# Performance work log

Measured on AMD Instinct MI355X. Metric: run time of the kernel, lower is better.

## Reference

```python
import jax, jax.numpy as jnp
import numpy as np

B, N, D, H = 4, 1024, 512, 16
DH = D // H
FACTOR = 0.5 / np.sqrt(DH).astype(np.float32)


def setup_inputs() -> dict:
    key = jax.random.key(0)
    ks = jax.random.split(key, 16)
    w = lambda k, shape: (jax.random.normal(k, shape, dtype=jnp.float32) * 0.02)
    return {
        "H": jax.random.normal(ks[0], (B, N, D), dtype=jnp.float32),
        "V": jax.random.normal(ks[1], (B, N, 3, D), dtype=jnp.float32),
        "D_batch": jax.random.normal(ks[2], (B, N, N), dtype=jnp.float32),
        "rbf_feat": jax.random.normal(ks[3], (1, B, H, N, N), dtype=jnp.float32),
        "H_mask": jax.random.randint(ks[4], (B, N), 0, 2).astype(jnp.int32),
        "Wq": w(ks[5], (4 * D, D)), "bq": w(ks[6], (4 * D,)),
        "Wk": w(ks[7], (4 * D, D)), "bk": w(ks[8], (4 * D,)),
        "Wv": w(ks[9], (D, D)), "bv": w(ks[10], (D,)),
        "Wvv": w(ks[11], (D, D)),
        "Wo": w(ks[12], (D, D)), "bo": w(ks[13], (D,)),
        "Wvo": w(ks[14], (D, D)),
    }


def reference(H, V, D_batch, rbf_feat, H_mask, Wq, bq, Wk, bk, Wv, bv, Wvv, Wo, bo, Wvo):
    b, n, d = H.shape
    h = rbf_feat.shape[2]
    dh = d // h
    # projections
    H_q = (H @ Wq.T + bq).reshape(b, n, h, 4 * dh)
    H_k = (H @ Wk.T + bk).reshape(b, n, h, 4 * dh)
    H_v = (H @ Wv.T + bv).reshape(b, n, h, dh)
    # vector values: [b,n,3,d] -> [b,n,3,h,dh] -> [b,n,h,3,dh] -> [b,n,h,3*dh]
    V_v = jnp.einsum('bncd,ed->bnce', V, Wvv)
    V_v = jnp.swapaxes(V_v.reshape(b, n, 3, h, dh), -2, -3).reshape(b, n, h, 3 * dh)
    V_attn = jnp.concatenate([H_v, V_v], axis=-1)  # [b,n,h,4*dh]
    # additive bias + key mask
    bias = rbf_feat[0] + D_batch[:, None]            # [b,h,n,n]
    mask = (H_mask[:, None, None, :] != 0)           # [b,1,1,n]
    bias = jnp.where(mask, bias, -jnp.inf)
    scores = jnp.einsum('bnhd,bmhd->bhnm', H_q, H_k) * jnp.float32(FACTOR) + bias
    attn = jax.nn.softmax(scores, axis=-1)
    res = jnp.einsum('bhnm,bmhd->bnhd', attn, V_attn)  # [b,n,h,4*dh]
    H_res = res[..., :dh].reshape(b, n, d)
    V_res = jnp.swapaxes(res[..., dh:].reshape(b, n, h, 3, dh), -2, -3).reshape(b, n, 3, d)
    H_o = H_res @ Wo.T + bo
    V_o = jnp.einsum('bncd,ed->bnce', V_res, Wvo)
    return (H_o, V_o)
```

## Files before the change

### kernel.cpp

```cpp
#include <hip/hip_runtime.h>
#include <cmath>

#define FACTOR 0.08838834764831845f

typedef short s16x8 __attribute__((ext_vector_type(8)));
typedef float f32x4 __attribute__((ext_vector_type(4)));
typedef float f32x16 __attribute__((ext_vector_type(16)));
typedef unsigned int u32;

#define KEEP_LOADS() do { asm volatile("" ::: "memory"); __builtin_amdgcn_sched_barrier(0); } while (0)

__device__ __forceinline__ unsigned short f2bf(float x) {
  unsigned int u = __float_as_uint(x);
  u += 0x7FFFu + ((u >> 16) & 1u);
  return (unsigned short)(u >> 16);
}

__device__ __forceinline__ s16x8 pack8(float4 a, float4 b) {
  s16x8 r;
  r[0] = (short)f2bf(a.x); r[1] = (short)f2bf(a.y);
  r[2] = (short)f2bf(a.z); r[3] = (short)f2bf(a.w);
  r[4] = (short)f2bf(b.x); r[5] = (short)f2bf(b.y);
  r[6] = (short)f2bf(b.z); r[7] = (short)f2bf(b.w);
  return r;
}

__device__ __forceinline__ void gload_lds16(const void* g, void* l) {
  __builtin_amdgcn_global_load_lds(
      (const __attribute__((address_space(1))) u32*)g,
      (__attribute__((address_space(3))) u32*)l, 16, 0, 0);
}

__global__ __launch_bounds__(256) void gemm_mfma(
    const float* __restrict__ A, const float* __restrict__ B,
    const float* __restrict__ bias, void* __restrict__ C,
    int M, int N, int K, int mode)
{
  __shared__ unsigned short As[128 * 72];
  __shared__ unsigned short Bs[128 * 72];

  const int tid = threadIdx.x;
  const int w = tid >> 6, lane = tid & 63;
  const int l16 = lane & 15, lg = lane >> 4;
  const int wm = w >> 1, wn = w & 1;
  const int m0 = blockIdx.x * 128;
  const int n0 = blockIdx.y * 128;

  const int sr = tid >> 3;
  const int sc = (tid & 7) * 8;

  float4 ar[4][2], br[4][2];

  auto issue = [&](int k0) {
#pragma unroll
    for (int i = 0; i < 4; ++i) {
      const int rr = i * 32 + sr;
      const float* ap = A + (size_t)(m0 + rr) * K + k0 + sc;
      ar[i][0] = *(const float4*)ap;
      ar[i][1] = *(const float4*)(ap + 4);
      const float* bp;
      if (mode == 5) {
        const int t = n0 + rr;
        const int q3 = t >> 10, n = t & 1023;
        const int bb = q3 / 3, cd = q3 - 3 * bb;
        bp = B + (((size_t)(bb * 1024 + n)) * 3 + cd) * 512 + k0 + sc;
      } else {
        bp = B + (size_t)(n0 + rr) * K + k0 + sc;
      }
      br[i][0] = *(const float4*)bp;
      br[i][1] = *(const float4*)(bp + 4);
    }
  };

  f32x4 acc[4][4];
#pragma unroll
  for (int mt = 0; mt < 4; ++mt)
#pragma unroll
    for (int nt = 0; nt < 4; ++nt)
#pragma unroll
      for (int r = 0; r < 4; ++r) acc[mt][nt][r] = 0.f;

  issue(0);

#pragma unroll 1
  for (int k0 = 0; k0 < K; k0 += 64) {
    __builtin_amdgcn_s_barrier();
#pragma unroll
    for (int i = 0; i < 4; ++i) {
      const int rr = i * 32 + sr;
      *(s16x8*)&As[rr * 72 + sc] = pack8(ar[i][0], ar[i][1]);
      *(s16x8*)&Bs[rr * 72 + sc] = pack8(br[i][0], br[i][1]);
    }
    asm volatile("s_waitcnt lgkmcnt(0)" ::: "memory");
    __builtin_amdgcn_s_barrier();
    if (k0 + 64 < K) issue(k0 + 64);
    KEEP_LOADS();

#pragma unroll
    for (int ks = 0; ks < 2; ++ks) {
      s16x8 af[4], bf[4];
#pragma unroll
      for (int mt = 0; mt < 4; ++mt)
        af[mt] = *(const s16x8*)&As[(wm * 64 + mt * 16 + l16) * 72 + ks * 32 + lg * 8];
#pragma unroll
      for (int nt = 0; nt < 4; ++nt)
        bf[nt] = *(const s16x8*)&Bs[(wn * 64 + nt * 16 + l16) * 72 + ks * 32 + lg * 8];
#pragma unroll
      for (int mt = 0; mt < 4; ++mt)
#pragma unroll
        for (int nt = 0; nt < 4; ++nt)
          acc[mt][nt] = __builtin_amdgcn_mfma_f32_16x16x32_bf16(af[mt], bf[nt], acc[mt][nt], 0, 0, 0);
    }
  }

  const int rbase = m0 + wm * 64;
  const int cbase = n0 + wn * 64;

  if (mode == 0 || mode == 3) {
#pragma unroll
    for (int nt = 0; nt < 4; ++nt) {
      const int c = cbase + nt * 16 + l16;
      const float bb = bias ? bias[c] : 0.f;
#pragma unroll
      for (int mt = 0; mt < 4; ++mt) {
#pragma unroll
        for (int r = 0; r < 4; ++r) {
          const int row = rbase + mt * 16 + lg * 4 + r;
          const float v = acc[mt][nt][r] + bb;
          if (mode == 0) ((float*)C)[(size_t)row * N + c] = v;
          else           ((unsigned short*)C)[(size_t)row * N + c] = f2bf(v);
        }
      }
    }
  } else {
    unsigned short* Cb = (unsigned short*)C;
#pragma unroll
    for (int mt = 0; mt < 4; ++mt) {
#pragma unroll
      for (int r = 0; r < 4; ++r) {
        const int ch = rbase + mt * 16 + lg * 4 + r;
        const float bb = bias ? bias[ch] : 0.f;
        const int h = ch >> 5, dq = ch & 31;
#pragma unroll
        for (int nt = 0; nt < 4; ++nt) {
          const int t = cbase + nt * 16 + l16;
          size_t off;
          if (mode == 4) {
            const int b = t >> 10, n = t & 1023;
            off = (((size_t)(b * 16 + h)) * 128 + dq) * 1024 + n;
          } else {
            const int q3 = t >> 10, n = t & 1023;
            const int b = q3 / 3, cd = q3 - 3 * b;
            off = (((size_t)(b * 16 + h)) * 128 + 32 + cd * 32 + dq) * 1024 + n;
          }
          Cb[off] = f2bf(acc[mt][nt][r] + bb);
        }
      }
    }
  }
}

__global__ __launch_bounds__(256, 2) void attn_mfma(
    const unsigned short* __restrict__ Qg, const unsigned short* __restrict__ Kg,
    const unsigned short* __restrict__ Vtg, const float* __restrict__ rbf,
    const float* __restrict__ Dm, const int* __restrict__ msk,
    float* __restrict__ Hres, float* __restrict__ Vres)
{
  __shared__ unsigned short KsL[2][4096];
  __shared__ unsigned short VtL[2][4096];
  __shared__ int   MsL[1024];
  __shared__ float RbL[128 * 32];
  __shared__ float DbL[128 * 32];
  __shared__ float SsL[4][32 * 18];

  const int tid  = threadIdx.x;
  const int w    = tid >> 6;
  const int lane = tid & 63;
  const int l32  = lane & 31;
  const int hi   = lane >> 5;

  const int bh = blockIdx.y;
  const int b  = bh >> 4;
  const int h  = bh & 15;
  const int q0 = blockIdx.x * 128 + w * 32;

  s16x8 qf[8];
  {
    const unsigned short* qp = Qg + ((size_t)(b * 1024 + q0 + l32)) * 2048 + h * 128 + hi * 8;
#pragma unroll
    for (int ks = 0; ks < 8; ++ks) qf[ks] = *(const s16x8*)(qp + ks * 16);
  }

  f32x16 acc[4];
  float m_run = -INFINITY, l_run = 0.f;
#pragma unroll
  for (int dt = 0; dt < 4; ++dt)
#pragma unroll
    for (int r = 0; r < 16; ++r) acc[dt][r] = 0.f;

  auto issue_kv = [&](int t, int bf) {
    const int m0 = t * 32;
#pragma unroll
    for (int jj = 0; jj < 2; ++jj) {
      const int i = w * 2 + jj;
      gload_lds16(Kg + ((size_t)(b * 1024 + m0 + l32)) * 2048 + h * 128 + (2 * i + hi) * 8,
                  &KsL[bf][i * 512]);
      gload_lds16(Vtg + ((size_t)(bh * 128 + (i >> 1) * 32 + l32)) * 1024 + m0 + ((i & 1) * 2 + hi) * 8,
                  &VtL[bf][i * 512]);
    }
  };

  auto issue_bias = [&](int t) {
    const int m0 = t * 32;
#pragma unroll
    for (int i = 0; i < 4; ++i) {
      const int qq = q0 + i * 8 + (lane >> 3);
      const int ch = (lane & 7) * 4;
      gload_lds16(rbf + ((size_t)bh * 1024 + qq) * 1024 + m0 + ch, &RbL[w * 1024 + i * 256]);
      gload_lds16(Dm  + ((size_t)b  * 1024 + qq) * 1024 + m0 + ch, &DbL[w * 1024 + i * 256]);
    }
  };

  gload_lds16(msk + b * 1024 + w * 256 + lane * 4, &MsL[w * 256]);
  issue_kv(0, 0);
  issue_bias(0);

#pragma unroll 1
  for (int t = 0; t < 32; ++t) {
    const int bf = t & 1;
    const int m0 = t * 32;

    asm volatile("s_waitcnt vmcnt(0)" ::: "memory");
    __builtin_amdgcn_s_barrier();

    if (t < 31) issue_kv(t + 1, bf ^ 1);
    __builtin_amdgcn_sched_barrier(0);

    f32x16 sf;
#pragma unroll
    for (int r = 0; r < 16; ++r) sf[r] = 0.f;
    __builtin_amdgcn_s_setprio(1);
#pragma unroll
    for (int ks = 0; ks < 8; ++ks) {
      const s16x8 kf = *(const s16x8*)&KsL[bf][(ks * 2 + hi) * 256 + l32 * 8];
      sf = __builtin_amdgcn_mfma_f32_32x32x16_bf16(qf[ks], kf, sf, 0, 0, 0);
    }
    __builtin_amdgcn_s_setprio(0);

    const bool on = MsL[m0 + l32] != 0;
    float sv[16];
#pragma unroll
    for (int r = 0; r < 16; ++r) {
      const int ql = (r & 3) + 8 * (r >> 2) + 4 * hi;
      const float bb = RbL[w * 1024 + ql * 32 + l32] + DbL[w * 1024 + ql * 32 + l32];
      sv[r] = on ? fmaf(sf[r], FACTOR, bb) : -INFINITY;
    }
    asm volatile("s_waitcnt lgkmcnt(0)" ::: "memory");
    __builtin_amdgcn_sched_barrier(0);
    if (t < 31) issue_bias(t + 1);
    __builtin_amdgcn_sched_barrier(0);

    float s[16];
    if (l32 < 16) {
#pragma unroll
      for (int r = 0; r < 16; ++r) {
        const int ql = (r & 3) + 8 * (r >> 2) + 4 * hi;
        SsL[w][ql * 18 + l32] = sv[r];
      }
    }
    asm volatile("s_waitcnt lgkmcnt(0)" ::: "memory");
    __builtin_amdgcn_sched_barrier(0);
    if (hi == 0) {
#pragma unroll
      for (int j = 0; j < 16; ++j) s[j] = SsL[w][l32 * 18 + j];
    }
    __builtin_amdgcn_sched_barrier(0);
    if (l32 >= 16) {
#pragma unroll
      for (int r = 0; r < 16; ++r) {
        const int ql = (r & 3) + 8 * (r >> 2) + 4 * hi;
        SsL[w][ql * 18 + (l32 - 16)] = sv[r];
      }
    }
    asm volatile("s_waitcnt lgkmcnt(0)" ::: "memory");
    __builtin_amdgcn_sched_barrier(0);
    if (hi == 1) {
#pragma unroll
      for (int j = 0; j < 16; ++j) s[j] = SsL[w][l32 * 18 + j];
    }
    __builtin_amdgcn_sched_barrier(0);

    float mx = s[0];
#pragma unroll
    for (int j = 1; j < 16; ++j) mx = fmaxf(mx, s[j]);
    const float tmax = fmaxf(mx, __shfl_xor(mx, 32));

    const bool ok = (tmax <= m_run + 8.f);
    if (!__all(ok ? 1 : 0)) {
      const float mn = fmaxf(m_run, tmax);
      const float sc = (mn == m_run) ? 1.f : __expf(m_run - mn);
      m_run = mn;
      l_run *= sc;
#pragma unroll
      for (int dt = 0; dt < 4; ++dt)
#pragma unroll
        for (int r = 0; r < 16; ++r) acc[dt][r] *= sc;
    }

    float psv[16];
    float rs = 0.f;
#pragma unroll
    for (int j = 0; j < 16; ++j) {
      psv[j] = (s[j] == -INFINITY) ? 0.f : __expf(s[j] - m_run);
      rs += psv[j];
    }
    l_run += rs;

    {
      u32* Pw = (u32*)&SsL[w][0];
#pragma unroll
      for (int j = 0; j < 8; ++j) {
        const u32 word = (u32)f2bf(psv[2 * j]) | ((u32)f2bf(psv[2 * j + 1]) << 16);
        Pw[l32 * 18 + hi * 8 + j] = word;
      }
    }
    asm volatile("s_waitcnt lgkmcnt(0)" ::: "memory");
    __builtin_amdgcn_sched_barrier(0);

    const unsigned short* Pr = (const unsigned short*)&SsL[w][0];
    const s16x8 pf0 = *(const s16x8*)&Pr[l32 * 36 + hi * 8];
    const s16x8 pf1 = *(const s16x8*)&Pr[l32 * 36 + 16 + hi * 8];

    __builtin_amdgcn_s_setprio(1);
#pragma unroll
    for (int dt = 0; dt < 4; ++dt) {
      const s16x8 vf0 = *(const s16x8*)&VtL[bf][dt * 1024 + hi * 256 + l32 * 8];
      const s16x8 vf1 = *(const s16x8*)&VtL[bf][dt * 1024 + (2 + hi) * 256 + l32 * 8];
      acc[dt] = __builtin_amdgcn_mfma_f32_32x32x16_bf16(vf0, pf0, acc[dt], 0, 0, 0);
      acc[dt] = __builtin_amdgcn_mfma_f32_32x32x16_bf16(vf1, pf1, acc[dt], 0, 0, 0);
    }
    __builtin_amdgcn_s_setprio(0);
  }

  const float lt = l_run + __shfl_xor(l_run, 32);
  const float inv = (lt > 0.f) ? 1.f / lt : 0.f;

  const int q = q0 + l32;
#pragma unroll
  for (int dt = 0; dt < 4; ++dt) {
#pragma unroll
    for (int r = 0; r < 16; ++r) {
      const int dloc = (r & 3) + 8 * (r >> 2) + 4 * hi;
      const float o = acc[dt][r] * inv;
      if (dt == 0) {
        Hres[((size_t)(b * 1024 + q)) * 512 + h * 32 + dloc] = o;
      } else {
        Vres[(((size_t)(b * 1024 + q)) * 3 + (dt - 1)) * 512 + h * 32 + dloc] = o;
      }
    }
  }
}

extern "C" void kernel_launch(void* const* d_in, const int* in_sizes, int n_in,
                              void* d_out, int out_size, void* d_ws, size_t ws_size,
                              hipStream_t stream)
{
  const float* Hp  = (const float*)d_in[0];
  const float* Vp  = (const float*)d_in[1];
  const float* Db  = (const float*)d_in[2];
  const float* rbf = (const float*)d_in[3];
  const int*   Hm  = (const int*)d_in[4];
  const float* Wq  = (const float*)d_in[5];
  const float* bq  = (const float*)d_in[6];
  const float* Wk  = (const float*)d_in[7];
  const float* bk  = (const float*)d_in[8];
  const float* Wv  = (const float*)d_in[9];
  const float* bv  = (const float*)d_in[10];
  const float* Wvv = (const float*)d_in[11];
  const float* Wo  = (const float*)d_in[12];
  const float* bo  = (const float*)d_in[13];
  const float* Wvo = (const float*)d_in[14];
  float* out = (float*)d_out;

  if (ws_size < (size_t)83886080) return;
  unsigned short* Qb = (unsigned short*)d_ws;
  unsigned short* Kb = Qb + 8388608;
  unsigned short* Vt = Kb + 8388608;
  float* Hres = (float*)(Vt + 8388608);
  float* Vres = Hres + 2097152;

  const dim3 blk(256);

  gemm_mfma<<<dim3(32, 16), blk, 0, stream>>>(Hp, Wq, bq, Qb, 4096, 2048, 512, 3);
  gemm_mfma<<<dim3(32, 16), blk, 0, stream>>>(Hp, Wk, bk, Kb, 4096, 2048, 512, 3);
  gemm_mfma<<<dim3(4, 32),  blk, 0, stream>>>(Wv, Hp, bv, Vt, 512, 4096, 512, 4);
  gemm_mfma<<<dim3(4, 96),  blk, 0, stream>>>(Wvv, Vp, nullptr, Vt, 512, 12288, 512, 5);

  attn_mfma<<<dim3(8, 64), blk, 0, stream>>>(Qb, Kb, Vt, rbf, Db, Hm, Hres, Vres);

  gemm_mfma<<<dim3(32, 4), blk, 0, stream>>>(Hres, Wo, bo, out, 4096, 512, 512, 0);
  gemm_mfma<<<dim3(96, 4), blk, 0, stream>>>(Vres, Wvo, nullptr, out + 2097152, 12288, 512, 512, 0);
}
```

Before: 275.2 us.

## Pre-convert GEMM operands to bf16 and load tiles directly into LDS

Measured after the change: 307.6 us. 11.8% more time.

```diff
diff --git a/kernel.cpp b/kernel.cpp
--- a/kernel.cpp
+++ b/kernel.cpp
@@ -7,8 +7,6 @@
 typedef float f32x4 __attribute__((ext_vector_type(4)));
 typedef float f32x16 __attribute__((ext_vector_type(16)));
 typedef unsigned int u32;
-
-#define KEEP_LOADS() do { asm volatile("" ::: "memory"); __builtin_amdgcn_sched_barrier(0); } while (0)
 
 __device__ __forceinline__ unsigned short f2bf(float x) {
   unsigned int u = __float_as_uint(x);
@@ -31,13 +29,24 @@
       (__attribute__((address_space(3))) u32*)l, 16, 0, 0);
 }
 
-__global__ __launch_bounds__(256) void gemm_mfma(
-    const float* __restrict__ A, const float* __restrict__ B,
+__global__ __launch_bounds__(256) void cvt_bf16(
+    const float* __restrict__ src, unsigned short* __restrict__ dst, int n)
+{
+  const int i = (blockIdx.x * 256 + threadIdx.x) * 8;
+  if (i < n) {
+    const float4 a = *(const float4*)(src + i);
+    const float4 b = *(const float4*)(src + i + 4);
+    *(s16x8*)&dst[i] = pack8(a, b);
+  }
+}
+
+__global__ __launch_bounds__(256) void gemm_bf(
+    const unsigned short* __restrict__ A, const unsigned short* __restrict__ B,
     const float* __restrict__ bias, void* __restrict__ C,
     int M, int N, int K, int mode)
 {
-  __shared__ unsigned short As[128 * 72];
-  __shared__ unsigned short Bs[128 * 72];
+  __shared__ unsigned short ASl[8 * 1040];
+  __shared__ unsigned short BSl[8 * 1040];
 
   const int tid = threadIdx.x;
   const int w = tid >> 6, lane = tid & 63;
@@ -46,32 +55,6 @@
   const int m0 = blockIdx.x * 128;
   const int n0 = blockIdx.y * 128;
 
-  const int sr = tid >> 3;
-  const int sc = (tid & 7) * 8;
-
-  float4 ar[4][2], br[4][2];
-
-  auto issue = [&](int k0) {
-#pragma unroll
-    for (int i = 0; i < 4; ++i) {
-      const int rr = i * 32 + sr;
-      const float* ap = A + (size_t)(m0 + rr) * K + k0 + sc;
-      ar[i][0] = *(const float4*)ap;
-      ar[i][1] = *(const float4*)(ap + 4);
-      const float* bp;
-      if (mode == 5) {
-        const int t = n0 + rr;
-        const int q3 = t >> 10, n = t & 1023;
-        const int bb = q3 / 3, cd = q3 - 3 * bb;
-        bp = B + (((size_t)(bb * 1024 + n)) * 3 + cd) * 512 + k0 + sc;
-      } else {
-        bp = B + (size_t)(n0 + rr) * K + k0 + sc;
-      }
-      br[i][0] = *(const float4*)bp;
-      br[i][1] = *(const float4*)(bp + 4);
-    }
-  };
-
   f32x4 acc[4][4];
 #pragma unroll
   for (int mt = 0; mt < 4; ++mt)
@@ -79,32 +62,39 @@
     for (int nt = 0; nt < 4; ++nt)
 #pragma unroll
       for (int r = 0; r < 4; ++r) acc[mt][nt][r] = 0.f;
-
-  issue(0);
 
 #pragma unroll 1
   for (int k0 = 0; k0 < K; k0 += 64) {
     __builtin_amdgcn_s_barrier();
 #pragma unroll
     for (int i = 0; i < 4; ++i) {
-      const int rr = i * 32 + sr;
-      *(s16x8*)&As[rr * 72 + sc] = pack8(ar[i][0], ar[i][1]);
-      *(s16x8*)&Bs[rr * 72 + sc] = pack8(br[i][0], br[i][1]);
-    }
-    asm volatile("s_waitcnt lgkmcnt(0)" ::: "memory");
+      const int u = i * 256 + tid;
+      const int row = u & 127, ko = u >> 7;
+      const int dst = ko * 1040 + row * 8;
+      gload_lds16(A + (size_t)(m0 + row) * K + k0 + ko * 8, &ASl[dst]);
+      const unsigned short* bp;
+      if (mode == 5) {
+        const int t = n0 + row;
+        const int q3 = t >> 10, n = t & 1023;
+        const int bb = q3 / 3, cd = q3 - 3 * bb;
+        bp = B + (((size_t)(bb * 1024 + n)) * 3 + cd) * 512 + k0 + ko * 8;
+      } else {
+        bp = B + (size_t)(n0 + row) * K + k0 + ko * 8;
+      }
+      gload_lds16(bp, &BSl[dst]);
+    }
+    asm volatile("s_waitcnt vmcnt(0)" ::: "memory");
     __builtin_amdgcn_s_barrier();
-    if (k0 + 64 < K) issue(k0 + 64);
-    KEEP_LOADS();
 
 #pragma unroll
     for (int ks = 0; ks < 2; ++ks) {
       s16x8 af[4], bf[4];
 #pragma unroll
       for (int mt = 0; mt < 4; ++mt)
-        af[mt] = *(const s16x8*)&As[(wm * 64 + mt * 16 + l16) * 72 + ks * 32 + lg * 8];
+        af[mt] = *(const s16x8*)&ASl[(ks * 4 + lg) * 1040 + (wm * 64 + mt * 16 + l16) * 8];
 #pragma unroll
       for (int nt = 0; nt < 4; ++nt)
-        bf[nt] = *(const s16x8*)&Bs[(wn * 64 + nt * 16 + l16) * 72 + ks * 32 + lg * 8];
+        bf[nt] = *(const s16x8*)&BSl[(ks * 4 + lg) * 1040 + (wn * 64 + nt * 16 + l16) * 8];
 #pragma unroll
       for (int mt = 0; mt < 4; ++mt)
 #pragma unroll
@@ -164,7 +154,7 @@
     const unsigned short* __restrict__ Qg, const unsigned short* __restrict__ Kg,
     const unsigned short* __restrict__ Vtg, const float* __restrict__ rbf,
     const float* __restrict__ Dm, const int* __restrict__ msk,
-    float* __restrict__ Hres, float* __restrict__ Vres)
+    unsigned short* __restrict__ Hres, unsigned short* __restrict__ Vres)
 {
   __shared__ unsigned short KsL[2][4096];
   __shared__ unsigned short VtL[2][4096];
@@ -351,7 +341,7 @@
 #pragma unroll
     for (int r = 0; r < 16; ++r) {
       const int dloc = (r & 3) + 8 * (r >> 2) + 4 * hi;
-      const float o = acc[dt][r] * inv;
+      const unsigned short o = f2bf(acc[dt][r] * inv);
       if (dt == 0) {
         Hres[((size_t)(b * 1024 + q)) * 512 + h * 32 + dloc] = o;
       } else {
@@ -382,22 +372,39 @@
   const float* Wvo = (const float*)d_in[14];
   float* out = (float*)d_out;
 
-  if (ws_size < (size_t)83886080) return;
-  unsigned short* Qb = (unsigned short*)d_ws;
-  unsigned short* Kb = Qb + 8388608;
-  unsigned short* Vt = Kb + 8388608;
-  float* Hres = (float*)(Vt + 8388608);
-  float* Vres = Hres + 2097152;
+  if (ws_size < (size_t)90177536) return;
+  unsigned short* Qb    = (unsigned short*)d_ws;
+  unsigned short* Kb    = Qb + 8388608;
+  unsigned short* Vt    = Kb + 8388608;
+  unsigned short* HresB = Vt + 8388608;
+  unsigned short* VresB = HresB + 2097152;
+  unsigned short* Hb    = VresB + 6291456;
+  unsigned short* Vpb   = Hb + 2097152;
+  unsigned short* Wqb   = Vpb + 6291456;
+  unsigned short* Wkb   = Wqb + 1048576;
+  unsigned short* Wvb   = Wkb + 1048576;
+  unsigned short* Wvvb  = Wvb + 262144;
+  unsigned short* Wob   = Wvvb + 262144;
+  unsigned short* Wvob  = Wob + 262144;
 
   const dim3 blk(256);
 
-  gemm_mfma<<<dim3(32, 16), blk, 0, stream>>>(Hp, Wq, bq, Qb, 4096, 2048, 512, 3);
-  gemm_mfma<<<dim3(32, 16), blk, 0, stream>>>(Hp, Wk, bk, Kb, 4096, 2048, 512, 3);
-  gemm_mfma<<<dim3(4, 32),  blk, 0, stream>>>(Wv, Hp, bv, Vt, 512, 4096, 512, 4);
-  gemm_mfma<<<dim3(4, 96),  blk, 0, stream>>>(Wvv, Vp, nullptr, Vt, 512, 12288, 512, 5);
-
-  attn_mfma<<<dim3(8, 64), blk, 0, stream>>>(Qb, Kb, Vt, rbf, Db, Hm, Hres, Vres);
-
-  gemm_mfma<<<dim3(32, 4), blk, 0, stream>>>(Hres, Wo, bo, out, 4096, 512, 512, 0);
-  gemm_mfma<<<dim3(96, 4), blk, 0, stream>>>(Vres, Wvo, nullptr, out + 2097152, 12288, 512, 512, 0);
-}
+  cvt_bf16<<<dim3(1024), blk, 0, stream>>>(Hp,  Hb,   2097152);
+  cvt_bf16<<<dim3(3072), blk, 0, stream>>>(Vp,  Vpb,  6291456);
+  cvt_bf16<<<dim3(512),  blk, 0, stream>>>(Wq,  Wqb,  1048576);
+  cvt_bf16<<<dim3(512),  blk, 0, stream>>>(Wk,  Wkb,  1048576);
+  cvt_bf16<<<dim3(128),  blk, 0, stream>>>(Wv,  Wvb,  262144);
+  cvt_bf16<<<dim3(128),  blk, 0, stream>>>(Wvv, Wvvb, 262144);
+  cvt_bf16<<<dim3(128),  blk, 0, stream>>>(Wo,  Wob,  262144);
+  cvt_bf16<<<dim3(128),  blk, 0, stream>>>(Wvo, Wvob, 262144);
+
+  gemm_bf<<<dim3(32, 16), blk, 0, stream>>>(Hb, Wqb, bq, Qb, 4096, 2048, 512, 3);
+  gemm_bf<<<dim3(32, 16), blk, 0, stream>>>(Hb, Wkb, bk, Kb, 4096, 2048, 512, 3);
+  gemm_bf<<<dim3(4, 32),  blk, 0, stream>>>(Wvb, Hb, bv, Vt, 512, 4096, 512, 4);
+  gemm_bf<<<dim3(4, 96),  blk, 0, stream>>>(Wvvb, Vpb, nullptr, Vt, 512, 12288, 512, 5);
+
+  attn_mfma<<<dim3(8, 64), blk, 0, stream>>>(Qb, Kb, Vt, rbf, Db, Hm, HresB, VresB);
+
+  gemm_bf<<<dim3(32, 4), blk, 0, stream>>>(HresB, Wob, bo, out, 4096, 512, 512, 0);
+  gemm_bf<<<dim3(96, 4), blk, 0, stream>>>(VresB, Wvob, nullptr, out + 2097152, 12288, 512, 512, 0);
+}
```
